# Performance work log

Hardware: AMD Instinct MI355X
Metric: run time of the kernel (lower is better)

The kernel has to match this reference:

```python
import jax, jax.numpy as jnp
import numpy as np

# NaiveBias with bias_base_type='symmetric', has_bos=False, has_eos=False.
# w: (1, H, S) learned vector; expanded to symmetric Toeplitz bias (H, S, S),
# then contracted with v via einsum 'nlhd,nhlj->njhd' (bias pre-transposed in original).

def setup_inputs() -> dict:
    key = jax.random.key(0)
    k1, k2 = jax.random.split(key)
    B, S, H, D = 2, 2048, 16, 64
    v = jax.random.normal(k1, (B, S, H, D), dtype=jnp.float32)
    w = jax.random.normal(k2, (1, H, S), dtype=jnp.float32) * 0.02
    return {"v": v, "w": w}


def reference(v, w):
    B, S, H, D = v.shape  # no bos/eos -> seq_len == S, w_ sliced to [..., :S] (full w)
    # symmetric extension: w_ext[k] for k in [0, 2S-2], w_ext[S-1+r] = w[|r|]
    w_ext = jnp.concatenate([jnp.flip(w[..., 1:], axis=-1), w], axis=-1)  # (1, H, 2S-1)
    # original: bias[h, j, i] = w_ext[h, S-1-i+j]; transpose(0,1,3,2) -> bias_t[h, l, j] = w_ext[h, S-1-l+j]
    r = jnp.arange(S)
    idx = (S - 1) - r[:, None] + r[None, :]  # (S, S) Toeplitz index map
    bias_t = w_ext[0][:, idx]  # (H, S, S)
    # einsum 'nlhd,nhlj->njhd'; bias is identical across batch (repeat in _process is a copy)
    pbv = jnp.einsum('blhd,hlj->bjhd', v, bias_t)
    return pbv
```

## Files before the change

kernel.cpp:

```cpp
#include <hip/hip_runtime.h>
#include <stdint.h>


#define SS 2048
#define HH 16
#define BB 2
#define DD 64
#define BHN 32

typedef uint32_t u32;
typedef uint16_t u16;
typedef __attribute__((ext_vector_type(8))) short bf16x8;
typedef __attribute__((ext_vector_type(4))) float f32x4;

__device__ __forceinline__ u16 f2bf(float x) {
  u32 u = __float_as_uint(x);
  u = u + 0x7fffu + ((u >> 16) & 1u);
  return (u16)(u >> 16);
}
__device__ __forceinline__ float bf2f(u16 h) {
  return __uint_as_float(((u32)h) << 16);
}
__device__ __forceinline__ void bfsplit(float x, u16& hi, u16& lo) {
  hi = f2bf(x);
  lo = f2bf(x - bf2f(hi));
}

__global__ __launch_bounds__(256) void prep_v(const float* __restrict__ v,
                                              u16* __restrict__ vhi, u16* __restrict__ vlo)
{
  __shared__ float tile[64][68];
  const int t = threadIdx.x;
  const int l0 = blockIdx.x * 64;
  const int bh = blockIdx.y;
  const int b = bh >> 4, h = bh & 15;
  {
    const int lr = t >> 2, ds = (t & 3) * 16;
    const float* src = v + (((size_t)b * SS + l0 + lr) * HH + h) * DD + ds;
    float4 r0 = *(const float4*)(src + 0);
    float4 r1 = *(const float4*)(src + 4);
    float4 r2 = *(const float4*)(src + 8);
    float4 r3 = *(const float4*)(src + 12);
    *(float4*)&tile[lr][ds + 0]  = r0;
    *(float4*)&tile[lr][ds + 4]  = r1;
    *(float4*)&tile[lr][ds + 8]  = r2;
    *(float4*)&tile[lr][ds + 12] = r3;
  }
  __syncthreads();
  {
    const int d = t >> 2, lc = t & 3;
    union { u16 s[16]; uint4 q[2]; } ph, pl;
    #pragma unroll
    for (int i = 0; i < 16; ++i) {
      float x = tile[lc * 16 + i][d];
      u16 hi, lo; bfsplit(x, hi, lo);
      ph.s[i] = hi; pl.s[i] = lo;
    }
    u16* dh = vhi + (size_t)bh * (DD * SS) + (size_t)d * SS + l0 + lc * 16;
    u16* dl = vlo + (size_t)bh * (DD * SS) + (size_t)d * SS + l0 + lc * 16;
    *(uint4*)(dh + 0) = ph.q[0];
    *(uint4*)(dh + 8) = ph.q[1];
    *(uint4*)(dl + 0) = pl.q[0];
    *(uint4*)(dl + 8) = pl.q[1];
  }
}

__global__ __launch_bounds__(256) void prep_w(const float* __restrict__ w, u32* __restrict__ upk)
{
  const int h = blockIdx.x;
  const int t = blockIdx.y * 256 + threadIdx.x;
  int r = 2047 - t;
  int idx = r < 0 ? -r : r;
  if (idx > 2047) idx = 2047;
  float x = w[h * SS + idx];
  u16 hi, lo; bfsplit(x, hi, lo);
  upk[h * 4096 + t] = (u32)hi | ((u32)lo << 16);
}

__device__ __forceinline__ void load_afrag(const u32* tab, int t0, bf16x8& hi, bf16x8& lo) {
  u32 d0 = tab[t0 + 0], d1 = tab[t0 + 1], d2 = tab[t0 + 2], d3 = tab[t0 + 3];
  u32 d4 = tab[t0 + 4], d5 = tab[t0 + 5], d6 = tab[t0 + 6], d7 = tab[t0 + 7];
  union { u32 u[4]; bf16x8 v; } H, L;
  H.u[0] = __builtin_amdgcn_perm(d1, d0, 0x05040100u);
  H.u[1] = __builtin_amdgcn_perm(d3, d2, 0x05040100u);
  H.u[2] = __builtin_amdgcn_perm(d5, d4, 0x05040100u);
  H.u[3] = __builtin_amdgcn_perm(d7, d6, 0x05040100u);
  L.u[0] = __builtin_amdgcn_perm(d1, d0, 0x07060302u);
  L.u[1] = __builtin_amdgcn_perm(d3, d2, 0x07060302u);
  L.u[2] = __builtin_amdgcn_perm(d5, d4, 0x07060302u);
  L.u[3] = __builtin_amdgcn_perm(d7, d6, 0x07060302u);
  hi = H.v; lo = L.v;
}

__global__ __launch_bounds__(256) void toeplitz_mm(
    const u16* __restrict__ vhi, const u16* __restrict__ vlo,
    const u32* __restrict__ upk, float* __restrict__ out)
{
  __shared__ __align__(16) u32 tab[4096];
  __shared__ __align__(16) u16 vt[2][2][64][32];

  const int tid = threadIdx.x;
  const int lane = tid & 63;
  const int wv = tid >> 6;
  const int m = lane & 15;
  const int g = lane >> 4;

  const int lin = blockIdx.x + 8 * blockIdx.y;
  const int xcd = lin & 7;
  const int sl  = lin >> 3;
  const int bh  = (xcd << 2) | (sl >> 3);
  const int jt  = sl & 7;
  const int b = bh >> 4, h = bh & 15;

  {
    const u32* src = upk + h * 4096;
    #pragma unroll
    for (int r = 0; r < 4; ++r) {
      int idx = r * 1024 + tid * 4;
      *(uint4*)&tab[idx] = *(const uint4*)&src[idx];
    }
  }

  const int sd = tid >> 2;
  const int sg = tid & 3;
  const int sswz = (sd & 3) ^ ((sd >> 2) & 3);
  const int sp = sg ^ sswz;
  const u16* gvh = vhi + (size_t)bh * (DD * SS) + (size_t)sd * SS + sg * 8;
  const u16* gvl = vlo + (size_t)bh * (DD * SS) + (size_t)sd * SS + sg * 8;

  const int bswz = (m & 3) ^ ((m >> 2) & 3);
  const int boff = m * 32 + ((g ^ bswz) << 3);

  const int jb = jt * 256 + wv * 64;
  const int tA = 2047 - jb - m + 8 * g;

  {
    uint4 th = *(const uint4*)(gvh);
    uint4 tl = *(const uint4*)(gvl);
    *(uint4*)&vt[0][0][sd][sp * 8] = th;
    *(uint4*)&vt[0][1][sd][sp * 8] = tl;
  }
  __syncthreads();

  bf16x8 Ahi[4], Alo[4];
  #pragma unroll
  for (int jf = 0; jf < 4; ++jf)
    load_afrag(tab, tA - 16 * jf, Ahi[jf], Alo[jf]);

  f32x4 acc[4][4];
  #pragma unroll
  for (int i = 0; i < 4; ++i)
    #pragma unroll
    for (int j = 0; j < 4; ++j)
      acc[i][j] = (f32x4)(0.0f);

  int buf = 0;
  for (int s = 0; s < 64; ++s) {
    const int s1 = (s + 1) & 63;
    uint4 th = *(const uint4*)(gvh + s1 * 32);
    uint4 tl = *(const uint4*)(gvl + s1 * 32);

    const u16* vbh = &vt[buf][0][0][0];
    const u16* vbl = &vt[buf][1][0][0];
    #pragma unroll
    for (int nf = 0; nf < 4; ++nf) {
      bf16x8 bhf = *(const bf16x8*)(vbh + nf * 512 + boff);
      bf16x8 blf = *(const bf16x8*)(vbl + nf * 512 + boff);
      #pragma unroll
      for (int jf = 0; jf < 4; ++jf) {
        acc[jf][nf] = __builtin_amdgcn_mfma_f32_16x16x32_bf16(Ahi[jf], bhf, acc[jf][nf], 0, 0, 0);
        acc[jf][nf] = __builtin_amdgcn_mfma_f32_16x16x32_bf16(Ahi[jf], blf, acc[jf][nf], 0, 0, 0);
        acc[jf][nf] = __builtin_amdgcn_mfma_f32_16x16x32_bf16(Alo[jf], bhf, acc[jf][nf], 0, 0, 0);
      }
    }

    bf16x8 n0h, n0l, n1h, n1l;
    load_afrag(tab, tA + 32 * s1,      n0h, n0l);
    load_afrag(tab, tA + 32 * s1 - 16, n1h, n1l);
    Ahi[3] = Ahi[1]; Alo[3] = Alo[1];
    Ahi[2] = Ahi[0]; Alo[2] = Alo[0];
    Ahi[0] = n0h;    Alo[0] = n0l;
    Ahi[1] = n1h;    Alo[1] = n1l;

    *(uint4*)&vt[buf ^ 1][0][sd][sp * 8] = th;
    *(uint4*)&vt[buf ^ 1][1][sd][sp * 8] = tl;
    __syncthreads();
    buf ^= 1;
  }

  #pragma unroll
  for (int jf = 0; jf < 4; ++jf) {
    #pragma unroll
    for (int nf = 0; nf < 4; ++nf) {
      f32x4 c = acc[jf][nf];
      #pragma unroll
      for (int q = 0; q < 4; ++q) {
        int j = jb + jf * 16 + g * 4 + q;
        int d = nf * 16 + m;
        out[(((size_t)b * SS + j) * HH + h) * DD + d] = c[q];
      }
    }
  }
}

__global__ __launch_bounds__(256) void fallback_k(const float* __restrict__ v,
                                                  const float* __restrict__ w,
                                                  float* __restrict__ out)
{
  __shared__ float wrow[SS];
  const int t = threadIdx.x;
  const int j0 = blockIdx.x * 64;
  const int bh = blockIdx.y;
  const int b = bh >> 4, h = bh & 15;
  for (int i = t; i < SS; i += 256) wrow[i] = w[h * SS + i];
  __syncthreads();
  const int jj = t >> 6, d = t & 63;
  float acc[16];
  #pragma unroll
  for (int r = 0; r < 16; ++r) acc[r] = 0.f;
  for (int l = 0; l < SS; ++l) {
    float vv = v[(((size_t)b * SS + l) * HH + h) * DD + d];
    #pragma unroll
    for (int r = 0; r < 16; ++r) {
      int dj = l - (j0 + jj * 16 + r);
      acc[r] += wrow[dj < 0 ? -dj : dj] * vv;
    }
  }
  #pragma unroll
  for (int r = 0; r < 16; ++r)
    out[(((size_t)b * SS + (j0 + jj * 16 + r)) * HH + h) * DD + d] = acc[r];
}

extern "C" void kernel_launch(void* const* d_in, const int* in_sizes, int n_in,
                              void* d_out, int out_size, void* d_ws, size_t ws_size,
                              hipStream_t stream)
{
  const float* v = (const float*)d_in[0];
  const float* w = (const float*)d_in[1];
  float* out = (float*)d_out;
  const size_t vh_elems = (size_t)BHN * DD * SS;
  const size_t need = vh_elems * 4 + (size_t)HH * 4096 * 4;
  if (ws_size >= need) {
    u16* vhi = (u16*)d_ws;
    u16* vlo = vhi + vh_elems;
    u32* upk = (u32*)((char*)d_ws + vh_elems * 4);
    prep_v<<<dim3(32, 32), 256, 0, stream>>>(v, vhi, vlo);
    prep_w<<<dim3(16, 16), 256, 0, stream>>>(w, upk);
    toeplitz_mm<<<dim3(8, 32), 256, 0, stream>>>(vhi, vlo, upk, out);
  } else {
    fallback_k<<<dim3(32, 32), 256, 0, stream>>>(v, w, out);
  }
}
```

Before: 129.9 us.

## Fuse v bf16 split into Toeplitz matmul with split-K across two half-blocks

Removes the separate prep_v pass that converted v into transposed bf16 hi/lo arrays. The matmul kernel now reads fp32 v directly, splits it into hi/lo in registers, and writes it into shared memory. Each block has 512 threads split into two halves, each covering half of the L reduction. The halves are combined through a shared-memory reduction before the output is written. This saves a global write and read of the converted v and one kernel launch, at the cost of strided uncoalesced fp32 loads, extra syncs and reduction overhead.

```diff
diff --git a/kernel.cpp b/kernel.cpp
--- a/kernel.cpp
+++ b/kernel.cpp
@@ -4,9 +4,7 @@
 
 #define SS 2048
 #define HH 16
-#define BB 2
 #define DD 64
-#define BHN 32
 
 typedef uint32_t u32;
 typedef uint16_t u16;
@@ -24,45 +22,6 @@
 __device__ __forceinline__ void bfsplit(float x, u16& hi, u16& lo) {
   hi = f2bf(x);
   lo = f2bf(x - bf2f(hi));
-}
-
-__global__ __launch_bounds__(256) void prep_v(const float* __restrict__ v,
-                                              u16* __restrict__ vhi, u16* __restrict__ vlo)
-{
-  __shared__ float tile[64][68];
-  const int t = threadIdx.x;
-  const int l0 = blockIdx.x * 64;
-  const int bh = blockIdx.y;
-  const int b = bh >> 4, h = bh & 15;
-  {
-    const int lr = t >> 2, ds = (t & 3) * 16;
-    const float* src = v + (((size_t)b * SS + l0 + lr) * HH + h) * DD + ds;
-    float4 r0 = *(const float4*)(src + 0);
-    float4 r1 = *(const float4*)(src + 4);
-    float4 r2 = *(const float4*)(src + 8);
-    float4 r3 = *(const float4*)(src + 12);
-    *(float4*)&tile[lr][ds + 0]  = r0;
-    *(float4*)&tile[lr][ds + 4]  = r1;
-    *(float4*)&tile[lr][ds + 8]  = r2;
-    *(float4*)&tile[lr][ds + 12] = r3;
-  }
-  __syncthreads();
-  {
-    const int d = t >> 2, lc = t & 3;
-    union { u16 s[16]; uint4 q[2]; } ph, pl;
-    #pragma unroll
-    for (int i = 0; i < 16; ++i) {
-      float x = tile[lc * 16 + i][d];
-      u16 hi, lo; bfsplit(x, hi, lo);
-      ph.s[i] = hi; pl.s[i] = lo;
-    }
-    u16* dh = vhi + (size_t)bh * (DD * SS) + (size_t)d * SS + l0 + lc * 16;
-    u16* dl = vlo + (size_t)bh * (DD * SS) + (size_t)d * SS + l0 + lc * 16;
-    *(uint4*)(dh + 0) = ph.q[0];
-    *(uint4*)(dh + 8) = ph.q[1];
-    *(uint4*)(dl + 0) = pl.q[0];
-    *(uint4*)(dl + 8) = pl.q[1];
-  }
 }
 
 __global__ __launch_bounds__(256) void prep_w(const float* __restrict__ w, u32* __restrict__ upk)
@@ -92,20 +51,22 @@
   hi = H.v; lo = L.v;
 }
 
-__global__ __launch_bounds__(256) void toeplitz_mm(
-    const u16* __restrict__ vhi, const u16* __restrict__ vlo,
-    const u32* __restrict__ upk, float* __restrict__ out)
+__global__ __launch_bounds__(512, 2) void toeplitz_fused(
+    const float* __restrict__ v, const u32* __restrict__ upk, float* __restrict__ out)
 {
   __shared__ __align__(16) u32 tab[4096];
-  __shared__ __align__(16) u16 vt[2][2][64][32];
-
-  const int tid = threadIdx.x;
+  __shared__ __align__(16) u16 vt[2][2][2][64][32];
+  __shared__ __align__(16) float red[2][64][16];
+
+  const int tid  = threadIdx.x;
   const int lane = tid & 63;
-  const int wv = tid >> 6;
-  const int m = lane & 15;
-  const int g = lane >> 4;
-
-  const int lin = blockIdx.x + 8 * blockIdx.y;
+  const int wv   = tid >> 6;
+  const int half = wv >> 2;
+  const int oct  = wv & 3;
+  const int m    = lane & 15;
+  const int g    = lane >> 4;
+
+  const int lin = blockIdx.x;
   const int xcd = lin & 7;
   const int sl  = lin >> 3;
   const int bh  = (xcd << 2) | (sl >> 3);
@@ -114,39 +75,26 @@
 
   {
     const u32* src = upk + h * 4096;
-    #pragma unroll
-    for (int r = 0; r < 4; ++r) {
-      int idx = r * 1024 + tid * 4;
-      *(uint4*)&tab[idx] = *(const uint4*)&src[idx];
-    }
-  }
-
-  const int sd = tid >> 2;
-  const int sg = tid & 3;
-  const int sswz = (sd & 3) ^ ((sd >> 2) & 3);
-  const int sp = sg ^ sswz;
-  const u16* gvh = vhi + (size_t)bh * (DD * SS) + (size_t)sd * SS + sg * 8;
-  const u16* gvl = vlo + (size_t)bh * (DD * SS) + (size_t)sd * SS + sg * 8;
-
-  const int bswz = (m & 3) ^ ((m >> 2) & 3);
-  const int boff = m * 32 + ((g ^ bswz) << 3);
-
-  const int jb = jt * 256 + wv * 64;
-  const int tA = 2047 - jb - m + 8 * g;
-
-  {
-    uint4 th = *(const uint4*)(gvh);
-    uint4 tl = *(const uint4*)(gvl);
-    *(uint4*)&vt[0][0][sd][sp * 8] = th;
-    *(uint4*)&vt[0][1][sd][sp * 8] = tl;
-  }
-  __syncthreads();
+    *(uint4*)&tab[tid * 4]        = *(const uint4*)&src[tid * 4];
+    *(uint4*)&tab[2048 + tid * 4] = *(const uint4*)&src[2048 + tid * 4];
+  }
+
+  const int sd = lane;
+  const int sslot = oct ^ ((sd >> 2) & 3);
+  u16* wb0 = &vt[half][0][0][sd][sslot * 8];
+  u16* wb1 = &vt[half][1][0][sd][sslot * 8];
+  const float* gsrc = v + (((size_t)b * SS + half * 1024 + oct * 8) * HH + h) * DD + sd;
+
+  const int bro = m * 32 + ((g ^ ((m >> 2) & 3)) << 3);
+
+  const int jb = jt * 256 + oct * 64;
+  const int tA = 2047 - jb - m + 8 * g + half * 1024;
+
+  float r[8];
+  #pragma unroll
+  for (int i = 0; i < 8; ++i) r[i] = gsrc[i * 1024];
 
   bf16x8 Ahi[4], Alo[4];
-  #pragma unroll
-  for (int jf = 0; jf < 4; ++jf)
-    load_afrag(tab, tA - 16 * jf, Ahi[jf], Alo[jf]);
-
   f32x4 acc[4][4];
   #pragma unroll
   for (int i = 0; i < 4; ++i)
@@ -154,18 +102,44 @@
     for (int j = 0; j < 4; ++j)
       acc[i][j] = (f32x4)(0.0f);
 
-  int buf = 0;
-  for (int s = 0; s < 64; ++s) {
-    const int s1 = (s + 1) & 63;
-    uint4 th = *(const uint4*)(gvh + s1 * 32);
-    uint4 tl = *(const uint4*)(gvl + s1 * 32);
-
-    const u16* vbh = &vt[buf][0][0][0];
-    const u16* vbl = &vt[buf][1][0][0];
+  for (int s = 0; s < 32; ++s) {
+    u32 ph[4], pl[4];
+    #pragma unroll
+    for (int i = 0; i < 4; ++i) {
+      u16 h0, l0, h1, l1;
+      bfsplit(r[2 * i], h0, l0);
+      bfsplit(r[2 * i + 1], h1, l1);
+      ph[i] = (u32)h0 | ((u32)h1 << 16);
+      pl[i] = (u32)l0 | ((u32)l1 << 16);
+    }
+    u16* wb = (s & 1) ? wb1 : wb0;
+    *(uint4*)wb          = *(const uint4*)ph;
+    *(uint4*)(wb + 2048) = *(const uint4*)pl;
+    __syncthreads();
+
+    if (s < 31) {
+      const float* gs = gsrc + (size_t)(s + 1) * 32 * 1024;
+      #pragma unroll
+      for (int i = 0; i < 8; ++i) r[i] = gs[i * 1024];
+    }
+
+    if (s == 0) {
+      #pragma unroll
+      for (int jf = 0; jf < 4; ++jf)
+        load_afrag(tab, tA - 16 * jf, Ahi[jf], Alo[jf]);
+    } else {
+      bf16x8 t0h = Ahi[0], t0l = Alo[0], t1h = Ahi[1], t1l = Alo[1];
+      load_afrag(tab, tA + 32 * s,      Ahi[0], Alo[0]);
+      load_afrag(tab, tA + 32 * s - 16, Ahi[1], Alo[1]);
+      Ahi[2] = t0h; Alo[2] = t0l;
+      Ahi[3] = t1h; Alo[3] = t1l;
+    }
+
+    const u16* vb = &vt[half][s & 1][0][0][0];
     #pragma unroll
     for (int nf = 0; nf < 4; ++nf) {
-      bf16x8 bhf = *(const bf16x8*)(vbh + nf * 512 + boff);
-      bf16x8 blf = *(const bf16x8*)(vbl + nf * 512 + boff);
+      bf16x8 bhf = *(const bf16x8*)(vb + nf * 512 + bro);
+      bf16x8 blf = *(const bf16x8*)(vb + 2048 + nf * 512 + bro);
       #pragma unroll
       for (int jf = 0; jf < 4; ++jf) {
         acc[jf][nf] = __builtin_amdgcn_mfma_f32_16x16x32_bf16(Ahi[jf], bhf, acc[jf][nf], 0, 0, 0);
@@ -173,32 +147,33 @@
         acc[jf][nf] = __builtin_amdgcn_mfma_f32_16x16x32_bf16(Alo[jf], bhf, acc[jf][nf], 0, 0, 0);
       }
     }
-
-    bf16x8 n0h, n0l, n1h, n1l;
-    load_afrag(tab, tA + 32 * s1,      n0h, n0l);
-    load_afrag(tab, tA + 32 * s1 - 16, n1h, n1l);
-    Ahi[3] = Ahi[1]; Alo[3] = Alo[1];
-    Ahi[2] = Ahi[0]; Alo[2] = Alo[0];
-    Ahi[0] = n0h;    Alo[0] = n0l;
-    Ahi[1] = n1h;    Alo[1] = n1l;
-
-    *(uint4*)&vt[buf ^ 1][0][sd][sp * 8] = th;
-    *(uint4*)&vt[buf ^ 1][1][sd][sp * 8] = tl;
     __syncthreads();
-    buf ^= 1;
   }
 
   #pragma unroll
   for (int jf = 0; jf < 4; ++jf) {
-    #pragma unroll
-    for (int nf = 0; nf < 4; ++nf) {
-      f32x4 c = acc[jf][nf];
-      #pragma unroll
-      for (int q = 0; q < 4; ++q) {
-        int j = jb + jf * 16 + g * 4 + q;
-        int d = nf * 16 + m;
-        out[(((size_t)b * SS + j) * HH + h) * DD + d] = c[q];
+    for (int p = 0; p < 2; ++p) {
+      if (half == 1 && (oct >> 1) == p) {
+        float* dst = &red[oct & 1][lane][0];
+        #pragma unroll
+        for (int nf = 0; nf < 4; ++nf)
+          *(f32x4*)(dst + nf * 4) = acc[jf][nf];
       }
+      __syncthreads();
+      if (half == 0 && (oct >> 1) == p) {
+        const float* sp = &red[oct & 1][lane][0];
+        #pragma unroll
+        for (int nf = 0; nf < 4; ++nf) {
+          f32x4 c = acc[jf][nf] + *(const f32x4*)(sp + nf * 4);
+          #pragma unroll
+          for (int q = 0; q < 4; ++q) {
+            int j = jb + jf * 16 + g * 4 + q;
+            int d = nf * 16 + m;
+            out[(((size_t)b * SS + j) * HH + h) * DD + d] = c[q];
+          }
+        }
+      }
+      __syncthreads();
     }
   }
 }
@@ -238,15 +213,11 @@
   const float* v = (const float*)d_in[0];
   const float* w = (const float*)d_in[1];
   float* out = (float*)d_out;
-  const size_t vh_elems = (size_t)BHN * DD * SS;
-  const size_t need = vh_elems * 4 + (size_t)HH * 4096 * 4;
+  const size_t need = (size_t)HH * 4096 * 4;
   if (ws_size >= need) {
-    u16* vhi = (u16*)d_ws;
-    u16* vlo = vhi + vh_elems;
-    u32* upk = (u32*)((char*)d_ws + vh_elems * 4);
-    prep_v<<<dim3(32, 32), 256, 0, stream>>>(v, vhi, vlo);
+    u32* upk = (u32*)d_ws;
     prep_w<<<dim3(16, 16), 256, 0, stream>>>(w, upk);
-    toeplitz_mm<<<dim3(8, 32), 256, 0, stream>>>(vhi, vlo, upk, out);
+    toeplitz_fused<<<dim3(256), 512, 0, stream>>>(v, upk, out);
   } else {
     fallback_k<<<dim3(32, 32), 256, 0, stream>>>(v, w, out);
   }
```

After: 113.4 us. 1.15x faster.
